# Optimization experiments

Measured on AMD Instinct MI355X. Metric: run time of the kernel, lower is better.

Reference implementation:

```python
import jax, jax.numpy as jnp
import numpy as np

ALPHA = 0.2  # LeakyReLU negative slope (init arg `alpha`)
N, F_IN, F_OUT = 8192, 512, 256


def setup_inputs() -> dict:
    key = jax.random.key(0)
    k1, k2, k3, k4 = jax.random.split(key, 4)
    x = jax.random.normal(k1, (N, F_IN), dtype=jnp.float32)
    adj = jax.random.randint(k2, (N, N), 0, 2, dtype=jnp.int32)
    W = jax.random.normal(k3, (F_IN, F_OUT), dtype=jnp.float32) * (1.0 / np.sqrt(F_IN))
    a = jax.random.normal(k4, (2 * F_OUT, 1), dtype=jnp.float32) * (1.0 / np.sqrt(F_IN))
    return {"x": x, "adj": adj, "W": W, "a": a}


def reference(x, adj, W, a):
    h = x @ W  # [N, F_OUT]
    f_out = W.shape[1]
    # e[i,j] = LeakyReLU(a1 . h_i + a2 . h_j); computed without the O(N^2*2F) concat
    f1 = h @ a[:f_out, 0]   # [N]
    f2 = h @ a[f_out:, 0]   # [N]
    s = f1[:, None] + f2[None, :]  # [N, N]
    e = jnp.where(s >= 0, s, ALPHA * s)
    # Faithful to the source bug: -9e15 * zeros_like == zeros, so masked entries are 0.0
    att = jnp.where(adj > 0, e, jnp.zeros((), dtype=e.dtype))
    att = jax.nn.softmax(att, axis=1)
    # dropout is identity in eval mode
    h_prime = att @ h  # [N, F_OUT]
    return jax.nn.elu(h_prime)  # concat=True branch
```

## Files before the change

### kernel.cpp

```cpp
#include <hip/hip_runtime.h>
#include <stdint.h>

#define NN 8192
#define FIN 512
#define FOUT 256
#define ALPHA 0.2f
#define KSPLIT 4

typedef float f32x4 __attribute__((ext_vector_type(4)));
typedef short s16x8 __attribute__((ext_vector_type(8)));

__device__ __forceinline__ uint16_t f2bf(float f) {
  union { float f; uint32_t u; } v; v.f = f;
  uint32_t u = v.u + 0x7fffu + ((v.u >> 16) & 1u);
  return (uint16_t)(u >> 16);
}

__global__ __launch_bounds__(256) void k_wa(const float* __restrict__ W,
                                            const float* __restrict__ a,
                                            float* __restrict__ wa1, float* __restrict__ wa2) {
  __shared__ float a1[256], a2[256];
  int tid = threadIdx.x;
  a1[tid] = a[tid];
  a2[tid] = a[tid + 256];
  __syncthreads();
  int m = blockIdx.x * 256 + tid;
  const float* wrow = W + (size_t)m * FOUT;
  float s1 = 0.f, s2 = 0.f;
  for (int k = 0; k < FOUT; k += 4) {
    f32x4 v = *(const f32x4*)(wrow + k);
#pragma unroll
    for (int i = 0; i < 4; i++) {
      s1 += v[i] * a1[k + i];
      s2 += v[i] * a2[k + i];
    }
  }
  wa1[m] = s1; wa2[m] = s2;
}

__global__ __launch_bounds__(256) void k_f1f2(const float* __restrict__ x,
                                              const float* __restrict__ wa1,
                                              const float* __restrict__ wa2,
                                              float* __restrict__ f1, float* __restrict__ f2,
                                              float* __restrict__ l_arr) {
  __shared__ float s1[512], s2[512];
  int tid = threadIdx.x;
  if (tid < 4) l_arr[blockIdx.x * 4 + tid] = 0.f;
  s1[tid] = wa1[tid]; s1[tid + 256] = wa1[tid + 256];
  s2[tid] = wa2[tid]; s2[tid + 256] = wa2[tid + 256];
  __syncthreads();
  int w = tid >> 6, l = tid & 63;
  int row = blockIdx.x * 4 + w;
  const float* xr = x + (size_t)row * FIN + l * 8;
  f32x4 v0 = *(const f32x4*)xr;
  f32x4 v1 = *(const f32x4*)(xr + 4);
  int kb = l * 8;
  float d1 = 0.f, d2 = 0.f;
#pragma unroll
  for (int i = 0; i < 4; i++) {
    d1 += v0[i] * s1[kb + i] + v1[i] * s1[kb + 4 + i];
    d2 += v0[i] * s2[kb + i] + v1[i] * s2[kb + 4 + i];
  }
#pragma unroll
  for (int off = 32; off; off >>= 1) {
    d1 += __shfl_down(d1, off);
    d2 += __shfl_down(d2, off);
  }
  if (l == 0) { f1[row] = d1; f2[row] = d2; }
}

__global__ __launch_bounds__(256) void k_prep_wt(const float* __restrict__ W,
                                                 uint16_t* __restrict__ wt) {
  int idx = blockIdx.x * 256 + threadIdx.x;
  int f  = idx >> 7;
  int k4 = (idx & 127) * 4;
  ushort4 o;
  o.x = f2bf(W[(size_t)(k4 + 0) * FOUT + f]);
  o.y = f2bf(W[(size_t)(k4 + 1) * FOUT + f]);
  o.z = f2bf(W[(size_t)(k4 + 2) * FOUT + f]);
  o.w = f2bf(W[(size_t)(k4 + 3) * FOUT + f]);
  *(ushort4*)(wt + (size_t)f * FIN + k4) = o;
}

__global__ __launch_bounds__(256, 2) void k_gemm_h(const float* __restrict__ x,
                                                   const uint16_t* __restrict__ wt,
                                                   uint16_t* __restrict__ h) {
  __shared__ uint16_t Xs[64][40];
  __shared__ uint16_t Ws[128][40];
  int i0 = blockIdx.x * 64;
  int f0 = blockIdx.y * 128;
  int tid = threadIdx.x;
  int w = tid >> 6, l = tid & 63;
  int wr = w >> 1, wc = w & 1;
  int q = l >> 4, r16 = l & 15;
  f32x4 acc[2][4];
#pragma unroll
  for (int a = 0; a < 2; a++)
#pragma unroll
    for (int b = 0; b < 4; b++) acc[a][b] = (f32x4)0.f;

  int srow = tid >> 2, sch = tid & 3;
  for (int k0 = 0; k0 < FIN; k0 += 32) {
    const float* xp = x + (size_t)(i0 + srow) * FIN + k0 + sch * 8;
    f32x4 u0 = *(const f32x4*)xp;
    f32x4 u1 = *(const f32x4*)(xp + 4);
    uint4 pk;
    pk.x = (uint32_t)f2bf(u0[0]) | ((uint32_t)f2bf(u0[1]) << 16);
    pk.y = (uint32_t)f2bf(u0[2]) | ((uint32_t)f2bf(u0[3]) << 16);
    pk.z = (uint32_t)f2bf(u1[0]) | ((uint32_t)f2bf(u1[1]) << 16);
    pk.w = (uint32_t)f2bf(u1[2]) | ((uint32_t)f2bf(u1[3]) << 16);
    *(uint4*)(&Xs[srow][sch * 8]) = pk;
#pragma unroll
    for (int r = 0; r < 2; r++) {
      int idx = tid + r * 256;
      int rr = idx >> 2, cc = idx & 3;
      uint4 vw = *(const uint4*)(wt + (size_t)(f0 + rr) * FIN + k0 + cc * 8);
      *(uint4*)(&Ws[rr][cc * 8]) = vw;
    }
    __syncthreads();
    s16x8 A[2], B[4];
#pragma unroll
    for (int a = 0; a < 2; a++) A[a] = *(const s16x8*)(&Xs[wr * 32 + a * 16 + r16][q * 8]);
#pragma unroll
    for (int b = 0; b < 4; b++) B[b] = *(const s16x8*)(&Ws[wc * 64 + b * 16 + r16][q * 8]);
#pragma unroll
    for (int a = 0; a < 2; a++)
#pragma unroll
      for (int b = 0; b < 4; b++)
        acc[a][b] = __builtin_amdgcn_mfma_f32_16x16x32_bf16(A[a], B[b], acc[a][b], 0, 0, 0);
    __syncthreads();
  }
#pragma unroll
  for (int a = 0; a < 2; a++)
#pragma unroll
    for (int b = 0; b < 4; b++)
#pragma unroll
      for (int reg = 0; reg < 4; reg++) {
        int row = i0 + wr * 32 + a * 16 + q * 4 + reg;
        int col = f0 + wc * 64 + b * 16 + r16;
        h[(size_t)row * FOUT + col] = f2bf(acc[a][b][reg]);
      }
}

__global__ __launch_bounds__(256) void k_transpose(const uint16_t* __restrict__ h,
                                                   uint16_t* __restrict__ ht) {
  __shared__ uint16_t T[64][72];
  int i0 = blockIdx.x * 64, f0 = blockIdx.y * 64;
  int tid = threadIdx.x;
#pragma unroll
  for (int p = 0; p < 2; p++) {
    int idx = tid + p * 256;
    int r = idx >> 3, c8 = idx & 7;
    uint4 v = *(const uint4*)(h + (size_t)(i0 + r) * FOUT + f0 + c8 * 8);
    *(uint4*)(&T[r][c8 * 8]) = v;
  }
  __syncthreads();
#pragma unroll
  for (int p = 0; p < 2; p++) {
    int idx = tid + p * 256;
    int fr = idx >> 3, ic8 = idx & 7;
    s16x8 v;
#pragma unroll
    for (int j = 0; j < 8; j++) v[j] = (short)T[ic8 * 8 + j][fr];
    *(s16x8*)(ht + (size_t)(f0 + fr) * NN + i0 + ic8 * 8) = v;
  }
}

__global__ __launch_bounds__(256, 2) void k_att(const int* __restrict__ adj,
                                                const uint16_t* __restrict__ ht,
                                                const float* __restrict__ f1,
                                                const float* __restrict__ f2,
                                                float* __restrict__ l_arr,
                                                float* __restrict__ part) {
  __shared__ uint16_t Ps[64][72];
  __shared__ uint16_t Hs[256][72];
  int i0 = blockIdx.x * 64;
  int jbase = blockIdx.y * (NN / KSPLIT);
  int tid = threadIdx.x;
  int w = tid >> 6, l = tid & 63;
  int q = l >> 4, r16 = l & 15;
  int prow = tid >> 2, pch = tid & 3;
  int srow = tid >> 3, sch = tid & 7;
  float f1i = f1[i0 + prow];
  float lsum = 0.f;
  f32x4 acc[4][4];
#pragma unroll
  for (int a = 0; a < 4; a++)
#pragma unroll
    for (int b = 0; b < 4; b++) acc[a][b] = (f32x4)0.f;

  for (int s = 0; s < NN / KSPLIT; s += 64) {
    int j0 = jbase + s;
    uint4 hv[8];
#pragma unroll
    for (int p = 0; p < 8; p++)
      hv[p] = *(const uint4*)(ht + (size_t)(p * 32 + srow) * NN + j0 + sch * 8);
    const int* ap = adj + (size_t)(i0 + prow) * NN + j0 + pch * 16;
    int4 A0 = *(const int4*)ap;
    int4 A1 = *(const int4*)(ap + 4);
    int4 A2 = *(const int4*)(ap + 8);
    int4 A3 = *(const int4*)(ap + 12);
    f32x4 F0 = *(const f32x4*)(f2 + j0 + pch * 16);
    f32x4 F1 = *(const f32x4*)(f2 + j0 + pch * 16 + 4);
    f32x4 F2 = *(const f32x4*)(f2 + j0 + pch * 16 + 8);
    f32x4 F3 = *(const f32x4*)(f2 + j0 + pch * 16 + 12);
    s16x8 pv0, pv1;
#define PCOMP(dst, Ac, Fc, kk) { float s_ = f1i + (Fc); float e_ = s_ > 0.f ? s_ : ALPHA * s_; \
                                 float p_ = ((Ac) != 0) ? __expf(e_) : 1.0f; lsum += p_; \
                                 dst[kk] = (short)f2bf(p_); }
    PCOMP(pv0, A0.x, F0[0], 0); PCOMP(pv0, A0.y, F0[1], 1);
    PCOMP(pv0, A0.z, F0[2], 2); PCOMP(pv0, A0.w, F0[3], 3);
    PCOMP(pv0, A1.x, F1[0], 4); PCOMP(pv0, A1.y, F1[1], 5);
    PCOMP(pv0, A1.z, F1[2], 6); PCOMP(pv0, A1.w, F1[3], 7);
    PCOMP(pv1, A2.x, F2[0], 0); PCOMP(pv1, A2.y, F2[1], 1);
    PCOMP(pv1, A2.z, F2[2], 2); PCOMP(pv1, A2.w, F2[3], 3);
    PCOMP(pv1, A3.x, F3[0], 4); PCOMP(pv1, A3.y, F3[1], 5);
    PCOMP(pv1, A3.z, F3[2], 6); PCOMP(pv1, A3.w, F3[3], 7);
#undef PCOMP
    *(s16x8*)(&Ps[prow][pch * 16]) = pv0;
    *(s16x8*)(&Ps[prow][pch * 16 + 8]) = pv1;
#pragma unroll
    for (int p = 0; p < 8; p++)
      *(uint4*)(&Hs[p * 32 + srow][sch * 8]) = hv[p];
    __syncthreads();
#pragma unroll
    for (int c = 0; c < 2; c++) {
      s16x8 Af[4], Bf[4];
#pragma unroll
      for (int a = 0; a < 4; a++) Af[a] = *(const s16x8*)(&Ps[a * 16 + r16][c * 32 + q * 8]);
#pragma unroll
      for (int b = 0; b < 4; b++) Bf[b] = *(const s16x8*)(&Hs[w * 64 + b * 16 + r16][c * 32 + q * 8]);
#pragma unroll
      for (int a = 0; a < 4; a++)
#pragma unroll
        for (int b = 0; b < 4; b++)
          acc[a][b] = __builtin_amdgcn_mfma_f32_16x16x32_bf16(Af[a], Bf[b], acc[a][b], 0, 0, 0);
    }
    __syncthreads();
  }

  lsum += __shfl_down(lsum, 2);
  lsum += __shfl_down(lsum, 1);
  if (pch == 0) atomicAdd(&l_arr[i0 + prow], lsum);

  float* pb = part + (size_t)blockIdx.y * ((size_t)NN * FOUT);
#pragma unroll
  for (int a = 0; a < 4; a++)
#pragma unroll
    for (int b = 0; b < 4; b++)
#pragma unroll
      for (int reg = 0; reg < 4; reg++) {
        int row = i0 + a * 16 + q * 4 + reg;
        int col = w * 64 + b * 16 + r16;
        pb[(size_t)row * FOUT + col] = acc[a][b][reg];
      }
}

__global__ __launch_bounds__(256) void k_combine(const float* __restrict__ part,
                                                 const float* __restrict__ l_arr,
                                                 float* __restrict__ out) {
  int idx = (blockIdx.x * 256 + threadIdx.x) * 4;
  float r = 1.0f / l_arr[idx >> 8];
  f32x4 v0 = *(const f32x4*)(part + 0 * (size_t)(NN * FOUT) + idx);
  f32x4 v1 = *(const f32x4*)(part + 1 * (size_t)(NN * FOUT) + idx);
  f32x4 v2 = *(const f32x4*)(part + 2 * (size_t)(NN * FOUT) + idx);
  f32x4 v3 = *(const f32x4*)(part + 3 * (size_t)(NN * FOUT) + idx);
  f32x4 o;
#pragma unroll
  for (int i = 0; i < 4; i++) {
    float v = (v0[i] + v1[i] + v2[i] + v3[i]) * r;
    o[i] = v > 0.f ? v : (__expf(v) - 1.f);
  }
  *(f32x4*)(out + idx) = o;
}

extern "C" void kernel_launch(void* const* d_in, const int* in_sizes, int n_in,
                              void* d_out, int out_size, void* d_ws, size_t ws_size,
                              hipStream_t stream) {
  const float* x   = (const float*)d_in[0];
  const int*   adj = (const int*)d_in[1];
  const float* W   = (const float*)d_in[2];
  const float* a   = (const float*)d_in[3];
  float* out = (float*)d_out;

  char* ws = (char*)d_ws;
  float*    wa1   = (float*)ws;
  float*    wa2   = wa1 + 512;
  float*    f1    = wa2 + 512;
  float*    f2    = f1 + NN;
  float*    l_arr = f2 + NN;
  uint16_t* wt    = (uint16_t*)(l_arr + NN);
  uint16_t* h     = wt + (size_t)FOUT * FIN;
  uint16_t* ht    = h + (size_t)NN * FOUT;
  float*    part  = (float*)(ht + (size_t)NN * FOUT);

  k_wa<<<2, 256, 0, stream>>>(W, a, wa1, wa2);
  k_f1f2<<<NN / 4, 256, 0, stream>>>(x, wa1, wa2, f1, f2, l_arr);
  k_prep_wt<<<128, 256, 0, stream>>>(W, wt);
  k_gemm_h<<<dim3(NN / 64, 2), 256, 0, stream>>>(x, wt, h);
  k_transpose<<<dim3(NN / 64, FOUT / 64), 256, 0, stream>>>(h, ht);
  k_att<<<dim3(NN / 64, KSPLIT), 256, 0, stream>>>(adj, ht, f1, f2, l_arr, part);
  k_combine<<<NN * FOUT / 1024, 256, 0, stream>>>(part, l_arr, out);
}
```

Before: 448.7 us.

## Fuse prep kernels, convert x to bf16 early, write h transposed, raise K-split

Merges the W-transpose and W·a kernels into one launch. The f1/f2 kernel now also writes a bf16 copy of x. The h GEMM is retiled to 64x64 and writes its output already transposed through shared memory, which removes the separate transpose kernel and the h round trip. KSPLIT rises from 4 to 8 to give the attention kernel more blocks, at the cost of twice the fp32 partial traffic in the combine step.

```diff
diff --git a/kernel.cpp b/kernel.cpp
--- a/kernel.cpp
+++ b/kernel.cpp
@@ -5,7 +5,7 @@
 #define FIN 512
 #define FOUT 256
 #define ALPHA 0.2f
-#define KSPLIT 4
+#define KSPLIT 8
 
 typedef float f32x4 __attribute__((ext_vector_type(4)));
 typedef short s16x8 __attribute__((ext_vector_type(8)));
@@ -16,32 +16,47 @@
   return (uint16_t)(u >> 16);
 }
 
-__global__ __launch_bounds__(256) void k_wa(const float* __restrict__ W,
-                                            const float* __restrict__ a,
-                                            float* __restrict__ wa1, float* __restrict__ wa2) {
-  __shared__ float a1[256], a2[256];
-  int tid = threadIdx.x;
-  a1[tid] = a[tid];
-  a2[tid] = a[tid + 256];
-  __syncthreads();
-  int m = blockIdx.x * 256 + tid;
-  const float* wrow = W + (size_t)m * FOUT;
-  float s1 = 0.f, s2 = 0.f;
-  for (int k = 0; k < FOUT; k += 4) {
-    f32x4 v = *(const f32x4*)(wrow + k);
-#pragma unroll
-    for (int i = 0; i < 4; i++) {
-      s1 += v[i] * a1[k + i];
-      s2 += v[i] * a2[k + i];
+__global__ __launch_bounds__(256) void k_wa_prep(const float* __restrict__ W,
+                                                 const float* __restrict__ a,
+                                                 uint16_t* __restrict__ wt,
+                                                 float* __restrict__ wa1, float* __restrict__ wa2) {
+  int bx = blockIdx.x;
+  int tid = threadIdx.x;
+  if (bx < 128) {
+    int idx = bx * 256 + tid;
+    int f  = idx >> 7;
+    int k4 = (idx & 127) * 4;
+    ushort4 o;
+    o.x = f2bf(W[(size_t)(k4 + 0) * FOUT + f]);
+    o.y = f2bf(W[(size_t)(k4 + 1) * FOUT + f]);
+    o.z = f2bf(W[(size_t)(k4 + 2) * FOUT + f]);
+    o.w = f2bf(W[(size_t)(k4 + 3) * FOUT + f]);
+    *(ushort4*)(wt + (size_t)f * FIN + k4) = o;
+  } else {
+    __shared__ float a1[256], a2[256];
+    a1[tid] = a[tid];
+    a2[tid] = a[tid + 256];
+    __syncthreads();
+    int m = (bx - 128) * 256 + tid;
+    const float* wrow = W + (size_t)m * FOUT;
+    float s1 = 0.f, s2 = 0.f;
+    for (int k = 0; k < FOUT; k += 4) {
+      f32x4 v = *(const f32x4*)(wrow + k);
+#pragma unroll
+      for (int i = 0; i < 4; i++) {
+        s1 += v[i] * a1[k + i];
+        s2 += v[i] * a2[k + i];
+      }
     }
-  }
-  wa1[m] = s1; wa2[m] = s2;
+    wa1[m] = s1; wa2[m] = s2;
+  }
 }
 
 __global__ __launch_bounds__(256) void k_f1f2(const float* __restrict__ x,
                                               const float* __restrict__ wa1,
                                               const float* __restrict__ wa2,
                                               float* __restrict__ f1, float* __restrict__ f2,
+                                              uint16_t* __restrict__ xb,
                                               float* __restrict__ l_arr) {
   __shared__ float s1[512], s2[512];
   int tid = threadIdx.x;
@@ -54,6 +69,12 @@
   const float* xr = x + (size_t)row * FIN + l * 8;
   f32x4 v0 = *(const f32x4*)xr;
   f32x4 v1 = *(const f32x4*)(xr + 4);
+  uint4 pk;
+  pk.x = (uint32_t)f2bf(v0[0]) | ((uint32_t)f2bf(v0[1]) << 16);
+  pk.y = (uint32_t)f2bf(v0[2]) | ((uint32_t)f2bf(v0[3]) << 16);
+  pk.z = (uint32_t)f2bf(v1[0]) | ((uint32_t)f2bf(v1[1]) << 16);
+  pk.w = (uint32_t)f2bf(v1[2]) | ((uint32_t)f2bf(v1[3]) << 16);
+  *(uint4*)(xb + (size_t)row * FIN + l * 8) = pk;
   int kb = l * 8;
   float d1 = 0.f, d2 = 0.f;
 #pragma unroll
@@ -69,91 +90,42 @@
   if (l == 0) { f1[row] = d1; f2[row] = d2; }
 }
 
-__global__ __launch_bounds__(256) void k_prep_wt(const float* __restrict__ W,
-                                                 uint16_t* __restrict__ wt) {
-  int idx = blockIdx.x * 256 + threadIdx.x;
-  int f  = idx >> 7;
-  int k4 = (idx & 127) * 4;
-  ushort4 o;
-  o.x = f2bf(W[(size_t)(k4 + 0) * FOUT + f]);
-  o.y = f2bf(W[(size_t)(k4 + 1) * FOUT + f]);
-  o.z = f2bf(W[(size_t)(k4 + 2) * FOUT + f]);
-  o.w = f2bf(W[(size_t)(k4 + 3) * FOUT + f]);
-  *(ushort4*)(wt + (size_t)f * FIN + k4) = o;
-}
-
-__global__ __launch_bounds__(256, 2) void k_gemm_h(const float* __restrict__ x,
-                                                   const uint16_t* __restrict__ wt,
-                                                   uint16_t* __restrict__ h) {
+__global__ __launch_bounds__(256, 2) void k_gemm_ht(const uint16_t* __restrict__ xb,
+                                                    const uint16_t* __restrict__ wt,
+                                                    uint16_t* __restrict__ ht) {
   __shared__ uint16_t Xs[64][40];
-  __shared__ uint16_t Ws[128][40];
+  __shared__ uint16_t Ws[64][40];
+  __shared__ uint16_t T[64][72];
   int i0 = blockIdx.x * 64;
-  int f0 = blockIdx.y * 128;
+  int f0 = blockIdx.y * 64;
   int tid = threadIdx.x;
   int w = tid >> 6, l = tid & 63;
-  int wr = w >> 1, wc = w & 1;
   int q = l >> 4, r16 = l & 15;
-  f32x4 acc[2][4];
-#pragma unroll
-  for (int a = 0; a < 2; a++)
-#pragma unroll
-    for (int b = 0; b < 4; b++) acc[a][b] = (f32x4)0.f;
+  f32x4 acc[4];
+#pragma unroll
+  for (int b = 0; b < 4; b++) acc[b] = (f32x4)0.f;
 
   int srow = tid >> 2, sch = tid & 3;
   for (int k0 = 0; k0 < FIN; k0 += 32) {
-    const float* xp = x + (size_t)(i0 + srow) * FIN + k0 + sch * 8;
-    f32x4 u0 = *(const f32x4*)xp;
-    f32x4 u1 = *(const f32x4*)(xp + 4);
-    uint4 pk;
-    pk.x = (uint32_t)f2bf(u0[0]) | ((uint32_t)f2bf(u0[1]) << 16);
-    pk.y = (uint32_t)f2bf(u0[2]) | ((uint32_t)f2bf(u0[3]) << 16);
-    pk.z = (uint32_t)f2bf(u1[0]) | ((uint32_t)f2bf(u1[1]) << 16);
-    pk.w = (uint32_t)f2bf(u1[2]) | ((uint32_t)f2bf(u1[3]) << 16);
-    *(uint4*)(&Xs[srow][sch * 8]) = pk;
-#pragma unroll
-    for (int r = 0; r < 2; r++) {
-      int idx = tid + r * 256;
-      int rr = idx >> 2, cc = idx & 3;
-      uint4 vw = *(const uint4*)(wt + (size_t)(f0 + rr) * FIN + k0 + cc * 8);
-      *(uint4*)(&Ws[rr][cc * 8]) = vw;
-    }
-    __syncthreads();
-    s16x8 A[2], B[4];
-#pragma unroll
-    for (int a = 0; a < 2; a++) A[a] = *(const s16x8*)(&Xs[wr * 32 + a * 16 + r16][q * 8]);
-#pragma unroll
-    for (int b = 0; b < 4; b++) B[b] = *(const s16x8*)(&Ws[wc * 64 + b * 16 + r16][q * 8]);
-#pragma unroll
-    for (int a = 0; a < 2; a++)
-#pragma unroll
-      for (int b = 0; b < 4; b++)
-        acc[a][b] = __builtin_amdgcn_mfma_f32_16x16x32_bf16(A[a], B[b], acc[a][b], 0, 0, 0);
-    __syncthreads();
-  }
-#pragma unroll
-  for (int a = 0; a < 2; a++)
+    uint4 xv = *(const uint4*)(xb + (size_t)(i0 + srow) * FIN + k0 + sch * 8);
+    uint4 wv = *(const uint4*)(wt + (size_t)(f0 + srow) * FIN + k0 + sch * 8);
+    *(uint4*)(&Xs[srow][sch * 8]) = xv;
+    *(uint4*)(&Ws[srow][sch * 8]) = wv;
+    __syncthreads();
+    s16x8 A = *(const s16x8*)(&Xs[w * 16 + r16][q * 8]);
+    s16x8 B[4];
+#pragma unroll
+    for (int b = 0; b < 4; b++) B[b] = *(const s16x8*)(&Ws[b * 16 + r16][q * 8]);
 #pragma unroll
     for (int b = 0; b < 4; b++)
-#pragma unroll
-      for (int reg = 0; reg < 4; reg++) {
-        int row = i0 + wr * 32 + a * 16 + q * 4 + reg;
-        int col = f0 + wc * 64 + b * 16 + r16;
-        h[(size_t)row * FOUT + col] = f2bf(acc[a][b][reg]);
-      }
-}
-
-__global__ __launch_bounds__(256) void k_transpose(const uint16_t* __restrict__ h,
-                                                   uint16_t* __restrict__ ht) {
-  __shared__ uint16_t T[64][72];
-  int i0 = blockIdx.x * 64, f0 = blockIdx.y * 64;
-  int tid = threadIdx.x;
-#pragma unroll
-  for (int p = 0; p < 2; p++) {
-    int idx = tid + p * 256;
-    int r = idx >> 3, c8 = idx & 7;
-    uint4 v = *(const uint4*)(h + (size_t)(i0 + r) * FOUT + f0 + c8 * 8);
-    *(uint4*)(&T[r][c8 * 8]) = v;
-  }
+      acc[b] = __builtin_amdgcn_mfma_f32_16x16x32_bf16(A, B[b], acc[b], 0, 0, 0);
+    __syncthreads();
+  }
+#pragma unroll
+  for (int b = 0; b < 4; b++)
+#pragma unroll
+    for (int reg = 0; reg < 4; reg++)
+      T[w * 16 + q * 4 + reg][b * 16 + r16] = f2bf(acc[b][reg]);
   __syncthreads();
 #pragma unroll
   for (int p = 0; p < 2; p++) {
@@ -261,14 +233,14 @@
                                                  float* __restrict__ out) {
   int idx = (blockIdx.x * 256 + threadIdx.x) * 4;
   float r = 1.0f / l_arr[idx >> 8];
-  f32x4 v0 = *(const f32x4*)(part + 0 * (size_t)(NN * FOUT) + idx);
-  f32x4 v1 = *(const f32x4*)(part + 1 * (size_t)(NN * FOUT) + idx);
-  f32x4 v2 = *(const f32x4*)(part + 2 * (size_t)(NN * FOUT) + idx);
-  f32x4 v3 = *(const f32x4*)(part + 3 * (size_t)(NN * FOUT) + idx);
+  f32x4 sum = (f32x4)0.f;
+#pragma unroll
+  for (int p = 0; p < KSPLIT; p++)
+    sum += *(const f32x4*)(part + (size_t)p * (NN * FOUT) + idx);
   f32x4 o;
 #pragma unroll
   for (int i = 0; i < 4; i++) {
-    float v = (v0[i] + v1[i] + v2[i] + v3[i]) * r;
+    float v = sum[i] * r;
     o[i] = v > 0.f ? v : (__expf(v) - 1.f);
   }
   *(f32x4*)(out + idx) = o;
@@ -290,15 +262,13 @@
   float*    f2    = f1 + NN;
   float*    l_arr = f2 + NN;
   uint16_t* wt    = (uint16_t*)(l_arr + NN);
-  uint16_t* h     = wt + (size_t)FOUT * FIN;
-  uint16_t* ht    = h + (size_t)NN * FOUT;
+  uint16_t* xb    = wt + (size_t)FOUT * FIN;
+  uint16_t* ht    = xb + (size_t)NN * FIN;
   float*    part  = (float*)(ht + (size_t)NN * FOUT);
 
-  k_wa<<<2, 256, 0, stream>>>(W, a, wa1, wa2);
-  k_f1f2<<<NN / 4, 256, 0, stream>>>(x, wa1, wa2, f1, f2, l_arr);
-  k_prep_wt<<<128, 256, 0, stream>>>(W, wt);
-  k_gemm_h<<<dim3(NN / 64, 2), 256, 0, stream>>>(x, wt, h);
-  k_transpose<<<dim3(NN / 64, FOUT / 64), 256, 0, stream>>>(h, ht);
+  k_wa_prep<<<130, 256, 0, stream>>>(W, a, wt, wa1, wa2);
+  k_f1f2<<<NN / 4, 256, 0, stream>>>(x, wa1, wa2, f1, f2, xb, l_arr);
+  k_gemm_ht<<<dim3(NN / 64, FOUT / 64), 256, 0, stream>>>(xb, wt, ht);
   k_att<<<dim3(NN / 64, KSPLIT), 256, 0, stream>>>(adj, ht, f1, f2, l_arr, part);
   k_combine<<<NN * FOUT / 1024, 256, 0, stream>>>(part, l_arr, out);
 }
```

New measurement: 464.0 us. 3.4% more time.
